# Kernel optimization log

Measured on AMD Instinct MI355X. Metric: run time of the kernel, lower is better.

## Reference

```python
import jax, jax.numpy as jnp
import numpy as np

DIM = 256
NUM_HEADS = 8
HEAD_DIM = DIM // NUM_HEADS


def _conv1x1(x, W, scale, bias):
    # 1x1 conv (bias=False) + eval-mode BN folded to per-channel scale/shift
    y = jnp.einsum('oc,bchw->bohw', W, x)
    return y * scale[None, :, None, None] + bias[None, :, None, None]


def setup_inputs() -> dict:
    key = jax.random.key(0)
    ks = jax.random.split(key, 16)
    B, H, W = 4, 64, 64
    Hu, Wu = 32, 32
    inp = {
        'x': jax.random.normal(ks[0], (B, DIM, H, W), jnp.float32),
        'upper_feat': jax.random.normal(ks[1], (B, DIM, Hu, Wu), jnp.float32),
        'Wq': jax.random.normal(ks[2], (DIM, DIM), jnp.float32) * 0.02,
        'q_scale': jax.random.uniform(ks[3], (DIM,), jnp.float32, 0.5, 1.5),
        'q_bias': jax.random.normal(ks[4], (DIM,), jnp.float32) * 0.02,
        'Wkv': jax.random.normal(ks[5], (2 * DIM, DIM), jnp.float32) * 0.02,
        'kv_scale': jax.random.uniform(ks[6], (2 * DIM,), jnp.float32, 0.5, 1.5),
        'kv_bias': jax.random.normal(ks[7], (2 * DIM,), jnp.float32) * 0.02,
        'Wpe': jax.random.normal(ks[8], (DIM, 1, 7, 7), jnp.float32) * 0.02,
        'pe_scale': jax.random.uniform(ks[9], (DIM,), jnp.float32, 0.5, 1.5),
        'pe_bias': jax.random.normal(ks[10], (DIM,), jnp.float32) * 0.02,
        'Wproj': jax.random.normal(ks[11], (DIM, DIM), jnp.float32) * 0.02,
        'proj_scale': jax.random.uniform(ks[12], (DIM,), jnp.float32, 0.5, 1.5),
        'proj_bias': jax.random.normal(ks[13], (DIM,), jnp.float32) * 0.02,
    }
    return inp


def reference(x, upper_feat, Wq, q_scale, q_bias, Wkv, kv_scale, kv_bias,
              Wpe, pe_scale, pe_bias, Wproj, proj_scale, proj_bias):
    B, C, H, W = x.shape
    N = H * W
    _, _, Hu, Wu = upper_feat.shape
    Nu = Hu * Wu

    # q branch: 1x1 conv+BN on x -> [B, heads, N, head_dim]
    q = _conv1x1(x, Wq, q_scale, q_bias)
    q = q.reshape(B, NUM_HEADS, HEAD_DIM, N).transpose(0, 1, 3, 2)

    # kv branch on upper (coarser) feature -> [B, heads, Nu, 2*head_dim]
    kv = _conv1x1(upper_feat, Wkv, kv_scale, kv_bias)
    kv = kv.reshape(B, NUM_HEADS, 2 * HEAD_DIM, Nu).transpose(0, 1, 3, 2)
    k, v = kv[..., :HEAD_DIM], kv[..., HEAD_DIM:]

    # cross attention: q over x pixels, k/v over upper pixels
    sim = jnp.einsum('bhnd,bhmd->bhnm', q, k) * (HEAD_DIM ** -0.5)
    attn = jax.nn.softmax(sim, axis=-1)
    ao = jnp.einsum('bhnm,bhmd->bhnd', attn, v)  # [B,h,N,hd]
    ao = ao.transpose(0, 1, 3, 2).reshape(B, C, H, W)

    # positional-encoding branch: depthwise 7x7 conv on v at upper resolution
    v_r = v.transpose(0, 1, 3, 2).reshape(B, C, Hu, Wu)
    v_pe = jax.lax.conv_general_dilated(
        v_r, Wpe, window_strides=(1, 1), padding=((3, 3), (3, 3)),
        feature_group_count=C,
        dimension_numbers=('NCHW', 'OIHW', 'NCHW'))
    v_pe = v_pe * pe_scale[None, :, None, None] + pe_bias[None, :, None, None]
    # bilinear upsample to x resolution (align_corners=False semantics)
    v_pe = jax.image.resize(v_pe, (B, C, H, W), method='bilinear')

    out = ao + v_pe
    return _conv1x1(out, Wproj, proj_scale, proj_bias)
```

## Files before the change

kernel.cpp:

```cpp
#include <hip/hip_runtime.h>
#include <hip/hip_bf16.h>

#define DIM 256
#define NHEADS 8
#define HDIM 32
#define Bq 4
#define Nq 4096
#define Nu 1024

typedef __attribute__((ext_vector_type(8))) short bf16x8;
typedef __attribute__((ext_vector_type(16))) float f32x16;
typedef __attribute__((ext_vector_type(4))) unsigned short us4;

__device__ __forceinline__ ushort f2bf(float x) {
    union { float f; unsigned u; } v; v.f = x;
    unsigned r = v.u + 0x7fffu + ((v.u >> 16) & 1u);
    return (ushort)(r >> 16);
}
__device__ __forceinline__ float bf2f(ushort u) {
    union { unsigned u; float f; } v; v.u = ((unsigned)u) << 16;
    return v.f;
}

__global__ __launch_bounds__(256) void prepro(
    const float* __restrict__ Wq, ushort* __restrict__ Oq,
    const float* __restrict__ Wkv, ushort* __restrict__ Okv,
    const float* __restrict__ Wp, ushort* __restrict__ Oph, ushort* __restrict__ Opl,
    const float* __restrict__ x, ushort* __restrict__ xT,
    const float* __restrict__ upper, ushort* __restrict__ upT)
{
    __shared__ ushort T[64][66];
    const int id = blockIdx.x;
    const int tid = threadIdx.x;

    if (id < 512) {
        int i = id * 256 + tid;
        if (i < 65536) {
            Oq[i] = f2bf(Wq[i]);
            float w = Wp[i];
            ushort h = f2bf(w);
            Oph[i] = h;
            Opl[i] = f2bf(w - bf2f(h));
        }
        Okv[i] = f2bf(Wkv[i]);
        return;
    }

    const float* In; ushort* OutT; int N, n0, c0, b;
    if (id < 1536) {
        int q = id - 512;
        In = x; OutT = xT; N = 4096;
        n0 = (q & 63) * 64; c0 = ((q >> 6) & 3) * 64; b = q >> 8;
    } else {
        int q = id - 1536;
        In = upper; OutT = upT; N = 1024;
        n0 = (q & 15) * 64; c0 = ((q >> 4) & 3) * 64; b = q >> 6;
    }

    const float* Ib = In + ((size_t)b * 256 + c0) * N + n0;
    const int nx = (tid & 15) * 4, cy = tid >> 4;
    #pragma unroll
    for (int p = 0; p < 4; ++p) {
        float4 v = *(const float4*)(Ib + (size_t)(cy + p * 16) * N + nx);
        T[nx + 0][cy + p * 16] = f2bf(v.x);
        T[nx + 1][cy + p * 16] = f2bf(v.y);
        T[nx + 2][cy + p * 16] = f2bf(v.z);
        T[nx + 3][cy + p * 16] = f2bf(v.w);
    }
    __syncthreads();
    ushort* Ob = OutT + ((size_t)b * N + n0) * 256 + c0;
    #pragma unroll
    for (int p = 0; p < 4; ++p) {
        int row = (tid >> 4) + p * 16;
        *(us4*)(Ob + (size_t)row * 256 + (tid & 15) * 4) = *(const us4*)&T[row][(tid & 15) * 4];
    }
}

__global__ __launch_bounds__(256, 4) void qkv_mfma(
    const ushort* __restrict__ Wqb, const ushort* __restrict__ xT,
    const float* __restrict__ q_scale, const float* __restrict__ q_bias, float qmult,
    const ushort* __restrict__ Wkvb, const ushort* __restrict__ upT,
    const float* __restrict__ kv_scale, const float* __restrict__ kv_bias,
    ushort* __restrict__ Qb, ushort* __restrict__ Kb, ushort* __restrict__ Vb)
{
    const int KD = 256;
    const int id = blockIdx.x;
    const int tid = threadIdx.x;
    const int w = tid >> 6, l = tid & 63;
    const int l31 = l & 31, hi = l >> 5;

    const ushort *Wb, *InT, *OutA; const float *scale, *bias;
    int N, n0, o0, b; float mult; bool isT; int bh;
    if (id < 512) {
        int q = id;
        int bx = q & 15, by = (q >> 4) & 7; b = q >> 7;
        N = 4096; n0 = (bx * 4 + w) * 64; o0 = by * 32;
        Wb = Wqb; InT = xT; scale = q_scale; bias = q_bias; mult = qmult;
        isT = true; bh = b * 8 + (o0 >> 5);
        OutA = Qb;
    } else {
        int q = id - 512;
        int bx = q & 3, by = (q >> 2) & 15; b = q >> 6;
        N = 1024; n0 = (bx * 4 + w) * 64; o0 = by * 32;
        Wb = Wkvb; InT = upT; scale = kv_scale; bias = kv_bias; mult = 1.0f;
        isT = ((o0 & 32) == 0); bh = b * 8 + (o0 >> 6);
        OutA = Kb;
    }

    const ushort* Wp = Wb + (size_t)(o0 + l31) * KD + hi * 8;
    const ushort* I0 = InT + ((size_t)b * N + n0 + l31) * KD + hi * 8;
    const ushort* I1 = I0 + (size_t)32 * KD;

    f32x16 acc0 = {}, acc1 = {};
    if (isT) {
        #pragma unroll 8
        for (int kk = 0; kk < KD; kk += 16) {
            bf16x8 wv = *(const bf16x8*)(Wp + kk);
            bf16x8 i0 = *(const bf16x8*)(I0 + kk);
            bf16x8 i1 = *(const bf16x8*)(I1 + kk);
            acc0 = __builtin_amdgcn_mfma_f32_32x32x16_bf16(i0, wv, acc0, 0, 0, 0);
            acc1 = __builtin_amdgcn_mfma_f32_32x32x16_bf16(i1, wv, acc1, 0, 0, 0);
        }
        const float sc = scale[o0 + l31] * mult;
        const float bi = bias[o0 + l31] * mult;
        ushort* Oa = (ushort*)OutA + ((size_t)bh * N) * 32 + l31;
        #pragma unroll
        for (int r = 0; r < 16; ++r) {
            const int dn = (r & 3) + 8 * (r >> 2) + 4 * hi;
            Oa[(size_t)(n0 + dn) * 32]      = f2bf(acc0[r] * sc + bi);
            Oa[(size_t)(n0 + 32 + dn) * 32] = f2bf(acc1[r] * sc + bi);
        }
    } else {
        #pragma unroll 8
        for (int kk = 0; kk < KD; kk += 16) {
            bf16x8 wv = *(const bf16x8*)(Wp + kk);
            bf16x8 i0 = *(const bf16x8*)(I0 + kk);
            bf16x8 i1 = *(const bf16x8*)(I1 + kk);
            acc0 = __builtin_amdgcn_mfma_f32_32x32x16_bf16(wv, i0, acc0, 0, 0, 0);
            acc1 = __builtin_amdgcn_mfma_f32_32x32x16_bf16(wv, i1, acc1, 0, 0, 0);
        }
        ushort* Ob = Vb + (size_t)bh * 32 * N;
        #pragma unroll
        for (int r = 0; r < 16; ++r) {
            const int dr = (r & 3) + 8 * (r >> 2) + 4 * hi;
            const float sc = scale[o0 + dr], bi = bias[o0 + dr];
            Ob[(size_t)dr * N + n0 + l31]      = f2bf(acc0[r] * sc + bi);
            Ob[(size_t)dr * N + n0 + 32 + l31] = f2bf(acc1[r] * sc + bi);
        }
    }
}

__global__ __launch_bounds__(256, 4) void attn_dw(
    const ushort* __restrict__ Qb, const ushort* __restrict__ Kt,
    const ushort* __restrict__ Vb, ushort* __restrict__ ao,
    const float* __restrict__ Wpe, const float* __restrict__ pe_scale,
    const float* __restrict__ pe_bias, ushort* __restrict__ vpe)
{
    __shared__ __align__(16) unsigned char smem[16384];
    const int tid = threadIdx.x;

    if (blockIdx.x < 1024) {
        const int w = tid >> 6, l = tid & 63;
        const int l31 = l & 31, hi = l >> 5;
        const int lid = blockIdx.x;
        const int j = lid >> 3;
        const int bh = (lid & 7) * 4 + (j >> 5);
        const int qbase = (j & 31) * 128 + w * 32;

        unsigned char (*ldsbuf)[8192] = (unsigned char(*)[8192])smem;

        const ushort* Qp = Qb + ((size_t)bh * 4096 + qbase) * 32;
        const unsigned char* Kg = (const unsigned char*)(Kt + (size_t)bh * 1024 * 32);
        const unsigned char* Vg = (const unsigned char*)(Vb + (size_t)bh * 32 * 1024);

        const bf16x8 qb0 = *(const bf16x8*)(Qp + (size_t)l31 * 32 + hi * 8);
        const bf16x8 qb1 = *(const bf16x8*)(Qp + (size_t)l31 * 32 + 16 + hi * 8);

        const int kr = tid >> 2, kc = tid & 3;
        const int vd = tid >> 3, vc = tid & 7;
        const int kwr = (kr * 64 + kc * 16) ^ ((kr & 7) << 4);
        const int vwr = vd * 128 + ((vc ^ (vd & 7)) << 4);

        f32x16 acc = {};
        float l_run = 0.f;

        uint4 kreg = *(const uint4*)(Kg + kr * 64 + kc * 16);
        uint4 vreg = *(const uint4*)(Vg + vd * 2048 + vc * 16);
        *(uint4*)(&ldsbuf[0][kwr]) = kreg;
        *(uint4*)(&ldsbuf[0][4096 + vwr]) = vreg;
        __syncthreads();

        for (int ph = 0; ph < 16; ++ph) {
            const int cur = ph & 1;
            if (ph < 15) {
                const size_t koff = (size_t)(ph + 1) * 4096;
                const int    voff = (ph + 1) * 128;
                kreg = *(const uint4*)(Kg + koff + kr * 64 + kc * 16);
                vreg = *(const uint4*)(Vg + (size_t)vd * 2048 + voff + vc * 16);
            }
            const unsigned char* Kl = &ldsbuf[cur][0];
            const unsigned char* Vl = &ldsbuf[cur][4096];

            #pragma unroll
            for (int s = 0; s < 2; ++s) {
                const int r = s * 32 + l31;
                bf16x8 ka0 = *(const bf16x8*)(Kl + ((r * 64 + hi * 16) ^ ((r & 7) << 4)));
                bf16x8 ka1 = *(const bf16x8*)(Kl + ((r * 64 + 32 + hi * 16) ^ ((r & 7) << 4)));
                bf16x8 va0 = *(const bf16x8*)(Vl + l31 * 128 + (((s * 4 + hi)     ^ (l31 & 7)) << 4));
                bf16x8 va1 = *(const bf16x8*)(Vl + l31 * 128 + (((s * 4 + 2 + hi) ^ (l31 & 7)) << 4));

                f32x16 sv = {};
                sv = __builtin_amdgcn_mfma_f32_32x32x16_bf16(ka0, qb0, sv, 0, 0, 0);
                sv = __builtin_amdgcn_mfma_f32_32x32x16_bf16(ka1, qb1, sv, 0, 0, 0);

                float p[16];
                #pragma unroll
                for (int r2 = 0; r2 < 16; ++r2) p[r2] = __builtin_amdgcn_exp2f(sv[r2]);
                l_run += (((p[0] + p[1]) + (p[2] + p[3])) + ((p[4] + p[5]) + (p[6] + p[7])))
                       + (((p[8] + p[9]) + (p[10] + p[11])) + ((p[12] + p[13]) + (p[14] + p[15])));

                int c[8];
                #pragma unroll
                for (int i = 0; i < 8; ++i)
                    asm("v_cvt_pk_bf16_f32 %0, %1, %2" : "=v"(c[i]) : "v"(p[2 * i]), "v"(p[2 * i + 1]));
                asm("v_permlane32_swap_b32 %0, %1" : "+v"(c[0]), "+v"(c[2]));
                asm("v_permlane32_swap_b32 %0, %1" : "+v"(c[1]), "+v"(c[3]));
                asm("v_permlane32_swap_b32 %0, %1" : "+v"(c[4]), "+v"(c[6]));
                asm("v_permlane32_swap_b32 %0, %1" : "+v"(c[5]), "+v"(c[7]));

                union { int i[4]; bf16x8 v; } b0u, b1u;
                b0u.i[0] = c[0]; b0u.i[1] = c[1]; b0u.i[2] = c[2]; b0u.i[3] = c[3];
                b1u.i[0] = c[4]; b1u.i[1] = c[5]; b1u.i[2] = c[6]; b1u.i[3] = c[7];

                acc = __builtin_amdgcn_mfma_f32_32x32x16_bf16(va0, b0u.v, acc, 0, 0, 0);
                acc = __builtin_amdgcn_mfma_f32_32x32x16_bf16(va1, b1u.v, acc, 0, 0, 0);
            }

            if (ph < 15) {
                const int nxt = cur ^ 1;
                *(uint4*)(&ldsbuf[nxt][kwr]) = kreg;
                *(uint4*)(&ldsbuf[nxt][4096 + vwr]) = vreg;
            }
            __syncthreads();
        }

        l_run += __shfl_xor(l_run, 32);
        float inv = 1.0f / l_run;

        ushort* aob = ao + ((size_t)(bh >> 3) * 256 + (bh & 7) * 32) * 4096 + qbase + l31;
        #pragma unroll
        for (int r = 0; r < 16; ++r) {
            const int d = (r & 3) + 8 * (r >> 2) + 4 * hi;
            aob[(size_t)d * 4096] = f2bf(acc[r] * inv);
        }
    } else {
        const int bc = blockIdx.x - 1024;
        const int b = bc >> 8, c = bc & 255;
        const ushort* vp = Vb + ((size_t)(b * 8 + (c >> 5)) * 32 + (c & 31)) * 1024;

        float* t   = (float*)smem;
        float* v32 = (float*)(smem + 5776);
        float* wl  = (float*)(smem + 9872);

        for (int i = tid; i < 38 * 38; i += 256) {
            int yy = i / 38 - 3, xx = i % 38 - 3;
            t[i] = (yy >= 0 && yy < 32 && xx >= 0 && xx < 32) ? bf2f(vp[yy * 32 + xx]) : 0.f;
        }
        if (tid < 49) wl[tid] = Wpe[(size_t)c * 49 + tid];
        __syncthreads();

        const float sc = pe_scale[c], bi = pe_bias[c];
        for (int i = tid; i < 1024; i += 256) {
            int y = i >> 5, x = i & 31;
            float s = 0.f;
            #pragma unroll
            for (int ky = 0; ky < 7; ++ky)
                #pragma unroll
                for (int kx = 0; kx < 7; ++kx)
                    s += t[(y + ky) * 38 + x + kx] * wl[ky * 7 + kx];
            v32[i] = s * sc + bi;
        }
        __syncthreads();

        ushort* op = vpe + (size_t)bc * 4096;
        #pragma unroll
        for (int p = 0; p < 16; ++p) {
            int idx = p * 256 + tid;
            int x = idx & 63, y = idx >> 6;
            float cx = x * 0.5f - 0.25f;
            float cy = y * 0.5f - 0.25f;
            int x0 = (x - 1) >> 1, y0 = (y - 1) >> 1;
            float fx = cx - x0, fy = cy - y0;
            int x0c = max(x0, 0), x1c = min(x0 + 1, 31);
            int y0c = max(y0, 0), y1c = min(y0 + 1, 31);
            float v00 = v32[y0c * 32 + x0c], v01 = v32[y0c * 32 + x1c];
            float v10 = v32[y1c * 32 + x0c], v11 = v32[y1c * 32 + x1c];
            float val = (1.f - fy) * ((1.f - fx) * v00 + fx * v01)
                      + fy * ((1.f - fx) * v10 + fx * v11);
            op[idx] = f2bf(val);
        }
    }
}

__global__ __launch_bounds__(256, 2) void proj_mfma(
    const ushort* __restrict__ Whi, const ushort* __restrict__ Wlo,
    const ushort* __restrict__ ao, const ushort* __restrict__ vpe,
    const float* __restrict__ scale, const float* __restrict__ bias,
    float* __restrict__ Out)
{
    __shared__ __align__(16) ushort S[64 * 256];
    const int tid = threadIdx.x;
    const int b  = blockIdx.z;
    const int n0 = blockIdx.x * 64;
    const int o0 = blockIdx.y * 128;

    {
        const int n8 = (tid & 7) * 8;
        const int c8 = (tid >> 3) * 8;
        const ushort* ap = ao  + ((size_t)b * 256 + c8) * 4096 + n0 + n8;
        const ushort* vp = vpe + ((size_t)b * 256 + c8) * 4096 + n0 + n8;
        unsigned ow[8][4];
        #pragma unroll
        for (int rp = 0; rp < 4; ++rp) {
            uint4 a0 = *(const uint4*)(ap + (size_t)(2 * rp) * 4096);
            uint4 a1 = *(const uint4*)(ap + (size_t)(2 * rp + 1) * 4096);
            uint4 v0 = *(const uint4*)(vp + (size_t)(2 * rp) * 4096);
            uint4 v1 = *(const uint4*)(vp + (size_t)(2 * rp + 1) * 4096);
            const unsigned* a0u = (const unsigned*)&a0;
            const unsigned* a1u = (const unsigned*)&a1;
            const unsigned* v0u = (const unsigned*)&v0;
            const unsigned* v1u = (const unsigned*)&v1;
            #pragma unroll
            for (int q = 0; q < 4; ++q) {
                float s0lo = __uint_as_float(a0u[q] << 16)
                           + __uint_as_float(v0u[q] << 16);
                float s0hi = __uint_as_float(a0u[q] & 0xffff0000u)
                           + __uint_as_float(v0u[q] & 0xffff0000u);
                float s1lo = __uint_as_float(a1u[q] << 16)
                           + __uint_as_float(v1u[q] << 16);
                float s1hi = __uint_as_float(a1u[q] & 0xffff0000u)
                           + __uint_as_float(v1u[q] & 0xffff0000u);
                unsigned plo, phi;
                asm("v_cvt_pk_bf16_f32 %0, %1, %2" : "=v"(plo) : "v"(s0lo), "v"(s1lo));
                asm("v_cvt_pk_bf16_f32 %0, %1, %2" : "=v"(phi) : "v"(s0hi), "v"(s1hi));
                ow[2 * q][rp]     = plo;
                ow[2 * q + 1][rp] = phi;
            }
        }
        #pragma unroll
        for (int j = 0; j < 8; ++j) {
            const int n = n8 + j;
            const int slot = (((c8 >> 3) ^ (n & 15)) & 31);
            *(uint4*)(&S[n * 256 + (slot << 3)]) = *(const uint4*)&ow[j][0];
        }
    }
    __syncthreads();

    const int w = tid >> 6, l = tid & 63;
    const int l31 = l & 31, hi = l >> 5;
    const int wo = w >> 1, wn = w & 1;
    const int ob = o0 + wo * 64;

    const ushort* wh0 = Whi + (size_t)(ob + l31) * 256 + hi * 8;
    const ushort* wh1 = wh0 + (size_t)32 * 256;
    const ushort* wl0 = Wlo + (size_t)(ob + l31) * 256 + hi * 8;
    const ushort* wl1 = wl0 + (size_t)32 * 256;

    const int nloc = wn * 32 + l31;
    const ushort* Srow = &S[nloc * 256];
    const int nsw = nloc & 15;

    f32x16 acc0 = {}, acc1 = {};
    #pragma unroll 4
    for (int kk = 0; kk < 256; kk += 16) {
        const int slot = (((kk >> 3) + hi) ^ nsw) & 31;
        bf16x8 av = *(const bf16x8*)(Srow + (slot << 3));
        bf16x8 h0 = *(const bf16x8*)(wh0 + kk);
        bf16x8 h1 = *(const bf16x8*)(wh1 + kk);
        bf16x8 g0 = *(const bf16x8*)(wl0 + kk);
        bf16x8 g1 = *(const bf16x8*)(wl1 + kk);
        acc0 = __builtin_amdgcn_mfma_f32_32x32x16_bf16(h0, av, acc0, 0, 0, 0);
        acc1 = __builtin_amdgcn_mfma_f32_32x32x16_bf16(h1, av, acc1, 0, 0, 0);
        acc0 = __builtin_amdgcn_mfma_f32_32x32x16_bf16(g0, av, acc0, 0, 0, 0);
        acc1 = __builtin_amdgcn_mfma_f32_32x32x16_bf16(g1, av, acc1, 0, 0, 0);
    }

    float* Ob = Out + (size_t)b * 256 * 4096 + n0 + wn * 32 + l31;
    #pragma unroll
    for (int r = 0; r < 16; ++r) {
        const int dr = (r & 3) + 8 * (r >> 2) + 4 * hi;
        const int oA = ob + dr, oB = ob + 32 + dr;
        Ob[(size_t)oA * 4096] = acc0[r] * scale[oA] + bias[oA];
        Ob[(size_t)oB * 4096] = acc1[r] * scale[oB] + bias[oB];
    }
}

extern "C" void kernel_launch(void* const* d_in, const int* in_sizes, int n_in,
                              void* d_out, int out_size, void* d_ws, size_t ws_size,
                              hipStream_t stream)
{
    const float* x        = (const float*)d_in[0];
    const float* upper    = (const float*)d_in[1];
    const float* Wq       = (const float*)d_in[2];
    const float* q_scale  = (const float*)d_in[3];
    const float* q_bias   = (const float*)d_in[4];
    const float* Wkv      = (const float*)d_in[5];
    const float* kv_scale = (const float*)d_in[6];
    const float* kv_bias  = (const float*)d_in[7];
    const float* Wpe      = (const float*)d_in[8];
    const float* pe_scale = (const float*)d_in[9];
    const float* pe_bias  = (const float*)d_in[10];
    const float* Wproj    = (const float*)d_in[11];
    const float* proj_scale = (const float*)d_in[12];
    const float* proj_bias  = (const float*)d_in[13];
    float* out = (float*)d_out;

    ushort* Qb   = (ushort*)d_ws;
    ushort* Kb   = Qb + (size_t)32 * 4096 * 32;
    ushort* Vb   = Kb + (size_t)32 * 1024 * 32;
    ushort* ao   = Vb + (size_t)32 * 1024 * 32;
    ushort* vpe  = ao + (size_t)Bq * DIM * Nq;
    ushort* Wqb  = vpe + (size_t)Bq * DIM * Nq;
    ushort* Wkvb = Wqb + 256 * 256;
    ushort* Wph  = Wkvb + 512 * 256;
    ushort* Wpl  = Wph + 256 * 256;
    ushort* xT   = ao;
    ushort* upT  = vpe;

    const float qmult = 0.17677669529663687f * 1.4426950408889634f;

    prepro<<<dim3(1792), 256, 0, stream>>>(Wq, Wqb, Wkv, Wkvb, Wproj, Wph, Wpl,
                                           x, xT, upper, upT);

    qkv_mfma<<<dim3(768), 256, 0, stream>>>(Wqb, xT, q_scale, q_bias, qmult,
                                            Wkvb, upT, kv_scale, kv_bias,
                                            Qb, Kb, Vb);

    attn_dw<<<dim3(2048), 256, 0, stream>>>(Qb, Kb, Vb, ao,
                                            Wpe, pe_scale, pe_bias, vpe);

    proj_mfma<<<dim3(64, 2, 4), 256, 0, stream>>>(Wph, Wpl, ao, vpe,
                                                  proj_scale, proj_bias, out);
}
```

Baseline: 88.80 us.

## Fuse input transpose and bf16 cast into QKV GEMM via swizzled LDS tile

Removes the separate transpose-and-convert pass over x and upper_feat from the prepro kernel. Each QKV block now loads its fp32 input tile directly, packs it to bf16 with v_cvt_pk_bf16_f32, and stores it into an XOR-swizzled shared-memory tile that all four waves reuse across output channels. K and V for a head are computed in the same block from one input tile. This saves a full bf16 write and re-read of both inputs, at the cost of repeated weight reads from global memory per block and an extra LDS staging step.

```diff
diff --git a/kernel.cpp b/kernel.cpp
--- a/kernel.cpp
+++ b/kernel.cpp
@@ -25,127 +25,128 @@
 __global__ __launch_bounds__(256) void prepro(
     const float* __restrict__ Wq, ushort* __restrict__ Oq,
     const float* __restrict__ Wkv, ushort* __restrict__ Okv,
-    const float* __restrict__ Wp, ushort* __restrict__ Oph, ushort* __restrict__ Opl,
-    const float* __restrict__ x, ushort* __restrict__ xT,
-    const float* __restrict__ upper, ushort* __restrict__ upT)
+    const float* __restrict__ Wp, ushort* __restrict__ Oph, ushort* __restrict__ Opl)
 {
-    __shared__ ushort T[64][66];
-    const int id = blockIdx.x;
-    const int tid = threadIdx.x;
-
-    if (id < 512) {
-        int i = id * 256 + tid;
-        if (i < 65536) {
-            Oq[i] = f2bf(Wq[i]);
-            float w = Wp[i];
-            ushort h = f2bf(w);
-            Oph[i] = h;
-            Opl[i] = f2bf(w - bf2f(h));
-        }
-        Okv[i] = f2bf(Wkv[i]);
-        return;
-    }
-
-    const float* In; ushort* OutT; int N, n0, c0, b;
-    if (id < 1536) {
-        int q = id - 512;
-        In = x; OutT = xT; N = 4096;
-        n0 = (q & 63) * 64; c0 = ((q >> 6) & 3) * 64; b = q >> 8;
-    } else {
-        int q = id - 1536;
-        In = upper; OutT = upT; N = 1024;
-        n0 = (q & 15) * 64; c0 = ((q >> 4) & 3) * 64; b = q >> 6;
-    }
-
-    const float* Ib = In + ((size_t)b * 256 + c0) * N + n0;
-    const int nx = (tid & 15) * 4, cy = tid >> 4;
-    #pragma unroll
-    for (int p = 0; p < 4; ++p) {
-        float4 v = *(const float4*)(Ib + (size_t)(cy + p * 16) * N + nx);
-        T[nx + 0][cy + p * 16] = f2bf(v.x);
-        T[nx + 1][cy + p * 16] = f2bf(v.y);
-        T[nx + 2][cy + p * 16] = f2bf(v.z);
-        T[nx + 3][cy + p * 16] = f2bf(v.w);
-    }
-    __syncthreads();
-    ushort* Ob = OutT + ((size_t)b * N + n0) * 256 + c0;
-    #pragma unroll
-    for (int p = 0; p < 4; ++p) {
-        int row = (tid >> 4) + p * 16;
-        *(us4*)(Ob + (size_t)row * 256 + (tid & 15) * 4) = *(const us4*)&T[row][(tid & 15) * 4];
-    }
+    const int i = blockIdx.x * 256 + threadIdx.x;
+    if (i < 65536) {
+        Oq[i] = f2bf(Wq[i]);
+        float w = Wp[i];
+        ushort h = f2bf(w);
+        Oph[i] = h;
+        Opl[i] = f2bf(w - bf2f(h));
+    }
+    Okv[i] = f2bf(Wkv[i]);
 }
 
 __global__ __launch_bounds__(256, 4) void qkv_mfma(
-    const ushort* __restrict__ Wqb, const ushort* __restrict__ xT,
+    const ushort* __restrict__ Wqb, const float* __restrict__ x,
     const float* __restrict__ q_scale, const float* __restrict__ q_bias, float qmult,
-    const ushort* __restrict__ Wkvb, const ushort* __restrict__ upT,
+    const ushort* __restrict__ Wkvb, const float* __restrict__ upper,
     const float* __restrict__ kv_scale, const float* __restrict__ kv_bias,
     ushort* __restrict__ Qb, ushort* __restrict__ Kb, ushort* __restrict__ Vb)
 {
-    const int KD = 256;
+    __shared__ __align__(16) ushort S[32 * 256];
     const int id = blockIdx.x;
     const int tid = threadIdx.x;
+
+    const float* In; int N, n0, b, oh; bool isQ;
+    if (id < 512) {
+        isQ = true; In = x; N = 4096;
+        n0 = (id & 127) * 32; b = id >> 7; oh = 0;
+    } else {
+        int q = id - 512;
+        isQ = false; In = upper; N = 1024;
+        n0 = (q & 31) * 32; oh = (q >> 5) & 1; b = q >> 6;
+    }
+
+    {
+        const int n4 = (tid & 7) * 4, c8 = (tid >> 3) * 8;
+        const float* ip = In + ((size_t)b * 256 + c8) * N + n0 + n4;
+        unsigned ow[4][4];
+        #pragma unroll
+        for (int rp = 0; rp < 4; ++rp) {
+            float4 f0 = *(const float4*)(ip + (size_t)(2 * rp) * N);
+            float4 f1 = *(const float4*)(ip + (size_t)(2 * rp + 1) * N);
+            asm("v_cvt_pk_bf16_f32 %0, %1, %2" : "=v"(ow[0][rp]) : "v"(f0.x), "v"(f1.x));
+            asm("v_cvt_pk_bf16_f32 %0, %1, %2" : "=v"(ow[1][rp]) : "v"(f0.y), "v"(f1.y));
+            asm("v_cvt_pk_bf16_f32 %0, %1, %2" : "=v"(ow[2][rp]) : "v"(f0.z), "v"(f1.z));
+            asm("v_cvt_pk_bf16_f32 %0, %1, %2" : "=v"(ow[3][rp]) : "v"(f0.w), "v"(f1.w));
+        }
+        #pragma unroll
+        for (int j = 0; j < 4; ++j) {
+            const int n = n4 + j;
+            const int slot = ((c8 >> 3) ^ (n & 15)) & 31;
+            *(uint4*)(&S[n * 256 + (slot << 3)]) = *(const uint4*)&ow[j][0];
+        }
+    }
+    __syncthreads();
+
     const int w = tid >> 6, l = tid & 63;
     const int l31 = l & 31, hi = l >> 5;
-
-    const ushort *Wb, *InT, *OutA; const float *scale, *bias;
-    int N, n0, o0, b; float mult; bool isT; int bh;
-    if (id < 512) {
-        int q = id;
-        int bx = q & 15, by = (q >> 4) & 7; b = q >> 7;
-        N = 4096; n0 = (bx * 4 + w) * 64; o0 = by * 32;
-        Wb = Wqb; InT = xT; scale = q_scale; bias = q_bias; mult = qmult;
-        isT = true; bh = b * 8 + (o0 >> 5);
-        OutA = Qb;
+    const int nsw = l31 & 15;
+    const ushort* Srow = &S[l31 * 256];
+
+    if (isQ) {
+        const ushort* w0 = Wqb + (size_t)(w * 64 + l31) * 256 + hi * 8;
+        const ushort* w1 = w0 + (size_t)32 * 256;
+        f32x16 acc0 = {}, acc1 = {};
+        #pragma unroll 8
+        for (int kk = 0; kk < 256; kk += 16) {
+            const int slot = (((kk >> 3) + hi) ^ nsw) & 31;
+            bf16x8 av = *(const bf16x8*)(Srow + (slot << 3));
+            bf16x8 h0 = *(const bf16x8*)(w0 + kk);
+            bf16x8 h1 = *(const bf16x8*)(w1 + kk);
+            acc0 = __builtin_amdgcn_mfma_f32_32x32x16_bf16(av, h0, acc0, 0, 0, 0);
+            acc1 = __builtin_amdgcn_mfma_f32_32x32x16_bf16(av, h1, acc1, 0, 0, 0);
+        }
+        #pragma unroll
+        for (int t = 0; t < 2; ++t) {
+            const f32x16 a = t ? acc1 : acc0;
+            const int orow = w * 64 + t * 32 + l31;
+            const float sc = q_scale[orow] * qmult;
+            const float bi = q_bias[orow] * qmult;
+            const int bh = b * 8 + 2 * w + t;
+            ushort* Oa = Qb + ((size_t)bh * 4096) * 32 + l31;
+            #pragma unroll
+            for (int r = 0; r < 16; ++r) {
+                const int dn = (r & 3) + 8 * (r >> 2) + 4 * hi;
+                Oa[(size_t)(n0 + dn) * 32] = f2bf(a[r] * sc + bi);
+            }
+        }
     } else {
-        int q = id - 512;
-        int bx = q & 3, by = (q >> 2) & 15; b = q >> 6;
-        N = 1024; n0 = (bx * 4 + w) * 64; o0 = by * 32;
-        Wb = Wkvb; InT = upT; scale = kv_scale; bias = kv_bias; mult = 1.0f;
-        isT = ((o0 & 32) == 0); bh = b * 8 + (o0 >> 6);
-        OutA = Kb;
-    }
-
-    const ushort* Wp = Wb + (size_t)(o0 + l31) * KD + hi * 8;
-    const ushort* I0 = InT + ((size_t)b * N + n0 + l31) * KD + hi * 8;
-    const ushort* I1 = I0 + (size_t)32 * KD;
-
-    f32x16 acc0 = {}, acc1 = {};
-    if (isT) {
+        const int h = oh * 4 + w;
+        const ushort* wk = Wkvb + (size_t)(h * 64 + l31) * 256 + hi * 8;
+        const ushort* wv = wk + (size_t)32 * 256;
+        f32x16 accK = {}, accV = {};
         #pragma unroll 8
-        for (int kk = 0; kk < KD; kk += 16) {
-            bf16x8 wv = *(const bf16x8*)(Wp + kk);
-            bf16x8 i0 = *(const bf16x8*)(I0 + kk);
-            bf16x8 i1 = *(const bf16x8*)(I1 + kk);
-            acc0 = __builtin_amdgcn_mfma_f32_32x32x16_bf16(i0, wv, acc0, 0, 0, 0);
-            acc1 = __builtin_amdgcn_mfma_f32_32x32x16_bf16(i1, wv, acc1, 0, 0, 0);
-        }
-        const float sc = scale[o0 + l31] * mult;
-        const float bi = bias[o0 + l31] * mult;
-        ushort* Oa = (ushort*)OutA + ((size_t)bh * N) * 32 + l31;
-        #pragma unroll
-        for (int r = 0; r < 16; ++r) {
-            const int dn = (r & 3) + 8 * (r >> 2) + 4 * hi;
-            Oa[(size_t)(n0 + dn) * 32]      = f2bf(acc0[r] * sc + bi);
-            Oa[(size_t)(n0 + 32 + dn) * 32] = f2bf(acc1[r] * sc + bi);
-        }
-    } else {
-        #pragma unroll 8
-        for (int kk = 0; kk < KD; kk += 16) {
-            bf16x8 wv = *(const bf16x8*)(Wp + kk);
-            bf16x8 i0 = *(const bf16x8*)(I0 + kk);
-            bf16x8 i1 = *(const bf16x8*)(I1 + kk);
-            acc0 = __builtin_amdgcn_mfma_f32_32x32x16_bf16(wv, i0, acc0, 0, 0, 0);
-            acc1 = __builtin_amdgcn_mfma_f32_32x32x16_bf16(wv, i1, acc1, 0, 0, 0);
-        }
-        ushort* Ob = Vb + (size_t)bh * 32 * N;
-        #pragma unroll
-        for (int r = 0; r < 16; ++r) {
-            const int dr = (r & 3) + 8 * (r >> 2) + 4 * hi;
-            const float sc = scale[o0 + dr], bi = bias[o0 + dr];
-            Ob[(size_t)dr * N + n0 + l31]      = f2bf(acc0[r] * sc + bi);
-            Ob[(size_t)dr * N + n0 + 32 + l31] = f2bf(acc1[r] * sc + bi);
+        for (int kk = 0; kk < 256; kk += 16) {
+            const int slot = (((kk >> 3) + hi) ^ nsw) & 31;
+            bf16x8 av = *(const bf16x8*)(Srow + (slot << 3));
+            bf16x8 k0 = *(const bf16x8*)(wk + kk);
+            bf16x8 v0 = *(const bf16x8*)(wv + kk);
+            accK = __builtin_amdgcn_mfma_f32_32x32x16_bf16(av, k0, accK, 0, 0, 0);
+            accV = __builtin_amdgcn_mfma_f32_32x32x16_bf16(v0, av, accV, 0, 0, 0);
+        }
+        const int bh = b * 8 + h;
+        {
+            const float sc = kv_scale[h * 64 + l31];
+            const float bi = kv_bias[h * 64 + l31];
+            ushort* Oa = Kb + ((size_t)bh * 1024) * 32 + l31;
+            #pragma unroll
+            for (int r = 0; r < 16; ++r) {
+                const int dn = (r & 3) + 8 * (r >> 2) + 4 * hi;
+                Oa[(size_t)(n0 + dn) * 32] = f2bf(accK[r] * sc + bi);
+            }
+        }
+        {
+            ushort* Ob = Vb + (size_t)bh * 32 * 1024;
+            #pragma unroll
+            for (int r = 0; r < 16; ++r) {
+                const int dr = (r & 3) + 8 * (r >> 2) + 4 * hi;
+                const float sc = kv_scale[h * 64 + 32 + dr];
+                const float bi = kv_bias[h * 64 + 32 + dr];
+                Ob[(size_t)dr * 1024 + n0 + l31] = f2bf(accV[r] * sc + bi);
+            }
         }
     }
 }
@@ -424,16 +425,13 @@
     ushort* Wkvb = Wqb + 256 * 256;
     ushort* Wph  = Wkvb + 512 * 256;
     ushort* Wpl  = Wph + 256 * 256;
-    ushort* xT   = ao;
-    ushort* upT  = vpe;
 
     const float qmult = 0.17677669529663687f * 1.4426950408889634f;
 
-    prepro<<<dim3(1792), 256, 0, stream>>>(Wq, Wqb, Wkv, Wkvb, Wproj, Wph, Wpl,
-                                           x, xT, upper, upT);
-
-    qkv_mfma<<<dim3(768), 256, 0, stream>>>(Wqb, xT, q_scale, q_bias, qmult,
-                                            Wkvb, upT, kv_scale, kv_bias,
+    prepro<<<dim3(512), 256, 0, stream>>>(Wq, Wqb, Wkv, Wkvb, Wproj, Wph, Wpl);
+
+    qkv_mfma<<<dim3(768), 256, 0, stream>>>(Wqb, x, q_scale, q_bias, qmult,
+                                            Wkvb, upper, kv_scale, kv_bias,
                                             Qb, Kb, Vb);
 
     attn_dw<<<dim3(2048), 256, 0, stream>>>(Qb, Kb, Vb, ao,
```

Result: faster. 82.47 us (-7.1%).
